# Kernel tuning notes

Hardware: AMD Instinct MI355X
Metric: run time of the kernel (lower is better)

## Reference

```python
import jax, jax.numpy as jnp
import numpy as np

COMMITMENT_COST = 0.25
EMBEDDING_DIM = 64
NUM_EMBEDDINGS = 512
BATCH, SEQ = 64, 4096


def setup_inputs() -> dict:
    key = jax.random.key(0)
    k1, k2, k3 = jax.random.split(key, 3)
    return {
        "inputs": jax.random.normal(k1, (BATCH, SEQ, EMBEDDING_DIM), dtype=jnp.float32),
        "embedding": jax.random.normal(k2, (NUM_EMBEDDINGS, EMBEDDING_DIM), dtype=jnp.float32),
        "ema_cluster_size": jax.random.uniform(k3, (NUM_EMBEDDINGS,), dtype=jnp.float32),
    }


def reference(inputs, embedding, ema_cluster_size):
    # inputs: [B, T, D]; embedding: [K, D]; ema_cluster_size: [K]
    input_shape = inputs.shape
    flat = inputs.reshape(-1, EMBEDDING_DIM)  # [N, D]
    distances = (
        jnp.sum(flat * flat, axis=1, keepdims=True)
        + jnp.sum(embedding * embedding, axis=1)[None, :]
        - 2.0 * (flat @ embedding.T)
    )
    # cluster-size weighting (as in the source module)
    distances = distances * jnp.sqrt(ema_cluster_size)[None, :]
    encoding_indices = jnp.argmin(distances, axis=1)  # [N]
    # one-hot @ codebook == gather
    quantized = embedding[encoding_indices].reshape(input_shape)
    e_latent_loss = jnp.mean((jax.lax.stop_gradient(quantized) - inputs) ** 2)
    loss = COMMITMENT_COST * e_latent_loss
    # straight-through estimator
    quantized_st = inputs + jax.lax.stop_gradient(quantized - inputs)
    return quantized_st, loss, encoding_indices[:, None]
```

## Files before the change

kernel.cpp:

```cpp
#include <hip/hip_runtime.h>
#include <math.h>

#define D 64
#define K 512

typedef __attribute__((ext_vector_type(8))) short short8;
typedef __attribute__((ext_vector_type(4))) float f32x4;

#define WS_E2    256
#define WS_SQ    2304
#define WS_ETS   4352
#define WS_BP    8448
#define WS_WL    139520
#define WS_PART  1188096
#define WS_PART2 1204480

#define KEYMASK 0xFFFFFE00u
#define DIST_BIAS 0.0625f

__device__ __forceinline__ unsigned short f32_to_bf16_rne(float f)
{
    unsigned int u = __float_as_uint(f);
    unsigned int r = (u + 0x7FFFu + ((u >> 16) & 1u)) >> 16;
    return (unsigned short)r;
}
__device__ __forceinline__ float bf16_to_f32(unsigned short h)
{
    return __uint_as_float(((unsigned int)h) << 16);
}

__device__ __forceinline__ float np_sumsq64(const float* v)
{
#pragma clang fp contract(off)
    float p[64];
#pragma unroll
    for (int i = 0; i < 64; ++i) p[i] = v[i] * v[i];
    float r[8];
#pragma unroll
    for (int j = 0; j < 8; ++j) r[j] = p[j];
#pragma unroll
    for (int b = 8; b < 64; b += 8) {
#pragma unroll
        for (int j = 0; j < 8; ++j) r[j] += p[b + j];
    }
    return ((r[0] + r[1]) + (r[2] + r[3])) + ((r[4] + r[5]) + (r[6] + r[7]));
}

__global__ __launch_bounds__(256) void vq_pack_prep(
    const float* __restrict__ emb,
    const float* __restrict__ cs,
    unsigned short* __restrict__ Bp,
    float* __restrict__ e2,
    float* __restrict__ sq,
    float2* __restrict__ ets,
    int* __restrict__ cnt)
{
    int i = blockIdx.x * blockDim.x + threadIdx.x;
    if (i < 65536) {
        int j    = i & 7;
        int lane = (i >> 3) & 63;
        int frag = (i >> 9) & 3;
        int t    = (i >> 11) & 31;
        int kc   = frag & 1;
        int sB   = frag >> 1;
        int code = t * 16 + (lane & 15);
        int d    = kc * 32 + (lane >> 4) * 8 + j;
        float v = emb[code * 64 + d];
        unsigned short b0 = f32_to_bf16_rne(v);
        Bp[i] = (sB == 0) ? b0 : f32_to_bf16_rne(v - bf16_to_f32(b0));
    } else if (i < 66048) {
        int k = i - 65536;
        float er[64];
        const float* ek = emb + (size_t)k * D;
#pragma unroll
        for (int d = 0; d < 64; ++d) er[d] = ek[d];
        float e2v = np_sumsq64(er);
        float sqv = (float)sqrt((double)cs[k]);
        e2[k] = e2v;
        sq[k] = sqv;
        ets[k] = make_float2(e2v * sqv + DIST_BIAS, 2.0f * sqv);
    } else if (i == 66048) {
        *cnt = 0;
    }
}

__global__ __launch_bounds__(256) void vq_screen(
    const float* __restrict__ x,
    const float* __restrict__ emb,
    const float2* __restrict__ ets,
    const unsigned short* __restrict__ Bp,
    float* __restrict__ out_q,
    float* __restrict__ out_idx,
    int* __restrict__ wl,
    int* __restrict__ cnt,
    double* __restrict__ partial)
{
    __shared__ double ls[4];

    const int wave = threadIdx.x >> 6;
    const int lane = threadIdx.x & 63;
    const int quad = lane >> 4;
    const int n16  = lane & 15;
    const int n0   = blockIdx.x * 128 + wave * 32;

    short8 A0[2][2], A1[2][2];
    float x2h[2][4];
#pragma unroll
    for (int rt = 0; rt < 2; ++rt) {
        float s = 0.0f;
#pragma unroll
        for (int kc = 0; kc < 2; ++kc) {
            const float* src = x + (size_t)(n0 + rt * 16 + n16) * 64
                               + kc * 32 + quad * 8;
            float4 v0 = *(const float4*)(src);
            float4 v1 = *(const float4*)(src + 4);
            float xv[8] = {v0.x, v0.y, v0.z, v0.w, v1.x, v1.y, v1.z, v1.w};
#pragma unroll
            for (int j = 0; j < 8; ++j) {
                float v = xv[j];
                unsigned short b0 = f32_to_bf16_rne(v);
                unsigned short b1 = f32_to_bf16_rne(v - bf16_to_f32(b0));
                A0[rt][kc][j] = (short)b0;
                A1[rt][kc][j] = (short)b1;
                s = fmaf(v, v, s);
            }
        }
        s += __shfl_xor(s, 16, 64);
        s += __shfl_xor(s, 32, 64);
#pragma unroll
        for (int r = 0; r < 4; ++r)
            x2h[rt][r] = 0.5f * __shfl(s, quad * 4 + r, 64);
    }

    unsigned k1[2][4], k2[2][4];
#pragma unroll
    for (int rt = 0; rt < 2; ++rt)
#pragma unroll
        for (int r = 0; r < 4; ++r) { k1[rt][r] = 0xFFFFFFFFu; k2[rt][r] = 0xFFFFFFFFu; }

#pragma unroll 2
    for (int t = 0; t < 32; ++t) {
        const unsigned short* bp = Bp + t * 2048 + lane * 8;
        const short8 B00 = *(const short8*)(bp);
        const short8 B01 = *(const short8*)(bp + 512);
        const short8 B10 = *(const short8*)(bp + 1024);
        const short8 B11 = *(const short8*)(bp + 1536);
        float2 et = ets[t * 16 + n16];
        unsigned cbits = (unsigned)(t * 16 + n16);

#pragma unroll
        for (int rt = 0; rt < 2; ++rt) {
            f32x4 acc = {0.0f, 0.0f, 0.0f, 0.0f};
            acc = __builtin_amdgcn_mfma_f32_16x16x32_bf16(A0[rt][0], B00, acc, 0, 0, 0);
            acc = __builtin_amdgcn_mfma_f32_16x16x32_bf16(A0[rt][1], B01, acc, 0, 0, 0);
            acc = __builtin_amdgcn_mfma_f32_16x16x32_bf16(A0[rt][0], B10, acc, 0, 0, 0);
            acc = __builtin_amdgcn_mfma_f32_16x16x32_bf16(A0[rt][1], B11, acc, 0, 0, 0);
            acc = __builtin_amdgcn_mfma_f32_16x16x32_bf16(A1[rt][0], B00, acc, 0, 0, 0);
            acc = __builtin_amdgcn_mfma_f32_16x16x32_bf16(A1[rt][1], B01, acc, 0, 0, 0);

#pragma unroll
            for (int r = 0; r < 4; ++r) {
                float dist = fmaf(x2h[rt][r], et.y, et.x);
                dist = fmaf(-et.y, acc[r], dist);
                unsigned key = (__float_as_uint(dist) & KEYMASK) | cbits;
                unsigned a1 = k1[rt][r];
                unsigned mx = a1 > key ? a1 : key;
                k1[rt][r] = a1 < key ? a1 : key;
                k2[rt][r] = k2[rt][r] < mx ? k2[rt][r] : mx;
            }
        }
    }

#pragma unroll
    for (int rt = 0; rt < 2; ++rt)
#pragma unroll
        for (int r = 0; r < 4; ++r) {
            unsigned a1 = k1[rt][r], a2 = k2[rt][r];
#pragma unroll
            for (int w = 1; w < 16; w <<= 1) {
                unsigned o1 = (unsigned)__shfl_xor((int)a1, w, 64);
                unsigned o2 = (unsigned)__shfl_xor((int)a2, w, 64);
                unsigned mx  = a1 > o1 ? a1 : o1;
                a1 = a1 < o1 ? a1 : o1;
                unsigned mn2 = a2 < o2 ? a2 : o2;
                a2 = mn2 < mx ? mn2 : mx;
            }
            k1[rt][r] = a1; k2[rt][r] = a2;
        }

    unsigned pk[2][4];
#pragma unroll
    for (int rt = 0; rt < 2; ++rt)
#pragma unroll
        for (int r = 0; r < 4; ++r) {
            float d1f = __uint_as_float(k1[rt][r] & KEYMASK);
            float d2f = __uint_as_float(k2[rt][r] & KEYMASK);
            int   i1  = (int)(k1[rt][r] & 0x1FFu);
            int   flg = (d2f - d1f) <= (0.01f + 2.0e-4f * d2f);
            pk[rt][r] = (unsigned)i1 | (flg ? 0x8000u : 0u);
            if (n16 == 0) {
                int p = n0 + rt * 16 + quad * 4 + r;
                out_idx[p] = (float)i1;
                if (flg) { int slot = atomicAdd(cnt, 1); wl[slot] = p; }
            }
        }

    int src = (n16 >> 2) * 16 + n16;
    double s = 0.0;
#pragma unroll
    for (int rt = 0; rt < 2; ++rt) {
        unsigned p0 = (unsigned)__shfl((int)pk[rt][0], src, 64);
        unsigned p1 = (unsigned)__shfl((int)pk[rt][1], src, 64);
        unsigned p2 = (unsigned)__shfl((int)pk[rt][2], src, 64);
        unsigned p3 = (unsigned)__shfl((int)pk[rt][3], src, 64);
        int rr = n16 & 3;
        unsigned pm = (rr == 0) ? p0 : (rr == 1) ? p1 : (rr == 2) ? p2 : p3;
        int bim = (int)(pm & 0x1FFu);
        int flg = (int)((pm >> 15) & 1u);
        if (!flg) {
            int prow = n0 + rt * 16 + n16;
#pragma unroll
            for (int kc = 0; kc < 2; ++kc) {
                const float* xs = x   + (size_t)prow * 64 + kc * 32 + quad * 8;
                const float* es = emb + (size_t)bim  * 64 + kc * 32 + quad * 8;
                float4 xv0 = *(const float4*)(xs);
                float4 xv1 = *(const float4*)(xs + 4);
                float4 ev0 = *(const float4*)(es);
                float4 ev1 = *(const float4*)(es + 4);
                float4 o0, o1;
                float t0, t1, t2, t3, t4, t5, t6, t7;
                {
#pragma clang fp contract(off)
                    t0 = ev0.x - xv0.x; o0.x = xv0.x + t0;
                    t1 = ev0.y - xv0.y; o0.y = xv0.y + t1;
                    t2 = ev0.z - xv0.z; o0.z = xv0.z + t2;
                    t3 = ev0.w - xv0.w; o0.w = xv0.w + t3;
                    t4 = ev1.x - xv1.x; o1.x = xv1.x + t4;
                    t5 = ev1.y - xv1.y; o1.y = xv1.y + t5;
                    t6 = ev1.z - xv1.z; o1.z = xv1.z + t6;
                    t7 = ev1.w - xv1.w; o1.w = xv1.w + t7;
                }
                float* od = out_q + (size_t)prow * 64 + kc * 32 + quad * 8;
                *(float4*)(od)     = o0;
                *(float4*)(od + 4) = o1;
                s += (double)t0 * t0 + (double)t1 * t1
                   + (double)t2 * t2 + (double)t3 * t3
                   + (double)t4 * t4 + (double)t5 * t5
                   + (double)t6 * t6 + (double)t7 * t7;
            }
        }
    }

#pragma unroll
    for (int off = 32; off > 0; off >>= 1)
        s += __shfl_down(s, off, 64);
    if (lane == 0) ls[wave] = s;
    __syncthreads();
    if (threadIdx.x == 0)
        partial[blockIdx.x] = ls[0] + ls[1] + ls[2] + ls[3];
}

__global__ __launch_bounds__(256) void vq_exact(
    const float* __restrict__ x,
    const float* __restrict__ emb,
    const float* __restrict__ e2,
    const float* __restrict__ sq,
    const int* __restrict__ wl,
    const int* __restrict__ cnt,
    float* __restrict__ out_idx,
    float* __restrict__ out_q,
    double* __restrict__ partial2)
{
    const int lane = threadIdx.x & 63;
    const int gw   = blockIdx.x * 4 + (threadIdx.x >> 6);
    const int nw   = gridDim.x * 4;
    const int cv   = *cnt;

    for (int w = gw; w < cv; w += nw) {
        int p = wl[w];
        const float* xrow = x + (size_t)p * 64;
        float row[64];
#pragma unroll
        for (int i = 0; i < 16; ++i) {
            float4 v = ((const float4*)xrow)[i];
            row[4 * i + 0] = v.x; row[4 * i + 1] = v.y;
            row[4 * i + 2] = v.z; row[4 * i + 3] = v.w;
        }
        float x2 = np_sumsq64(row);

        float bd = INFINITY;
        int   bc = 0;
        for (int t = 0; t < 8; ++t) {
            int c = t * 64 + lane;
            const float* er = emb + (size_t)c * 64;
            float acc = 0.0f;
#pragma unroll
            for (int d = 0; d < 64; ++d)
                acc = fmaf(row[d], er[d], acc);
            float dist;
            {
#pragma clang fp contract(off)
                dist = ((x2 + e2[c]) - 2.0f * acc) * sq[c];
            }
            if (dist < bd) { bd = dist; bc = c; }
        }
#pragma unroll
        for (int wd = 1; wd < 64; wd <<= 1) {
            float od = __shfl_xor(bd, wd, 64);
            int   oc = __shfl_xor(bc, wd, 64);
            if (od < bd || (od == bd && oc < bc)) { bd = od; bc = oc; }
        }
        if (lane == 0) out_idx[p] = (float)bc;

        float xv = x[(size_t)p * 64 + lane];
        float qv = emb[(size_t)bc * 64 + lane];
        float t, o;
        {
#pragma clang fp contract(off)
            t = qv - xv;
            o = xv + t;
        }
        out_q[(size_t)p * 64 + lane] = o;
        double dd = (double)t * (double)t;
#pragma unroll
        for (int off = 32; off > 0; off >>= 1)
            dd += __shfl_down(dd, off, 64);
        if (lane == 0) partial2[w] = dd;
    }
}

__global__ __launch_bounds__(256) void vq_finalize(
    const double* __restrict__ partial,
    const double* __restrict__ partial2,
    const int* __restrict__ cnt,
    float* __restrict__ loss_out,
    int nblk, double inv_count)
{
    double s = 0.0;
    for (int i = threadIdx.x; i < nblk; i += 256) s += partial[i];
    int cv = *cnt;
    for (int w = threadIdx.x; w < cv; w += 256) s += partial2[w];
#pragma unroll
    for (int off = 32; off > 0; off >>= 1)
        s += __shfl_down(s, off, 64);
    __shared__ double ls[4];
    if ((threadIdx.x & 63) == 0) ls[threadIdx.x >> 6] = s;
    __syncthreads();
    if (threadIdx.x == 0) {
        double total = ls[0] + ls[1] + ls[2] + ls[3];
        loss_out[0] = (float)(0.25 * total * inv_count);
    }
}

extern "C" void kernel_launch(void* const* d_in, const int* in_sizes, int n_in,
                              void* d_out, int out_size, void* d_ws, size_t ws_size,
                              hipStream_t stream)
{
    const float* x   = (const float*)d_in[0];
    const float* emb = (const float*)d_in[1];
    const float* cs  = (const float*)d_in[2];

    const int N = in_sizes[0] / D;

    float* out      = (float*)d_out;
    float* out_q    = out;
    float* out_loss = out + (size_t)N * D;
    float* out_idx  = out_loss + 1;

    char* ws = (char*)d_ws;
    int*            cnt      = (int*)ws;
    float*          e2       = (float*)(ws + WS_E2);
    float*          sq       = (float*)(ws + WS_SQ);
    float2*         ets      = (float2*)(ws + WS_ETS);
    unsigned short* Bp       = (unsigned short*)(ws + WS_BP);
    int*            wl       = (int*)(ws + WS_WL);
    double*         partial  = (double*)(ws + WS_PART);
    double*         partial2 = (double*)(ws + WS_PART2);

    const int nblk_screen = N / 128;

    vq_pack_prep<<<259, 256, 0, stream>>>(emb, cs, Bp, e2, sq, ets, cnt);
    vq_screen<<<nblk_screen, 256, 0, stream>>>(x, emb, ets, Bp,
                                               out_q, out_idx, wl, cnt, partial);
    vq_exact<<<512, 256, 0, stream>>>(x, emb, e2, sq, wl, cnt,
                                      out_idx, out_q, partial2);
    vq_finalize<<<1, 256, 0, stream>>>(partial, partial2, cnt, out_loss,
                                       nblk_screen, 1.0 / ((double)N * (double)D));
}
```

Baseline: 214.6 us.

## Stage packed codebook in LDS and process more rows per larger block

The screening kernel now copies the whole packed bf16 codebook (128 KB) into shared memory once per block and reads the MFMA B operands from LDS instead of global or L2. Blocks grow to 512 threads, each covering 512 rows in two passes, so the staging cost is amortised. It also seeds the accumulator with -x²/2 to drop one FMA and uses v_med3_u32 for the second-smallest key update. The 128 KB of LDS per block limits occupancy to one block per CU, and the staging copy plus barrier adds latency at the start of each block.

```diff
diff --git a/kernel.cpp b/kernel.cpp
--- a/kernel.cpp
+++ b/kernel.cpp
@@ -84,7 +84,7 @@
     }
 }
 
-__global__ __launch_bounds__(256) void vq_screen(
+__global__ __launch_bounds__(512) void vq_screen(
     const float* __restrict__ x,
     const float* __restrict__ emb,
     const float2* __restrict__ ets,
@@ -95,158 +95,173 @@
     int* __restrict__ cnt,
     double* __restrict__ partial)
 {
-    __shared__ double ls[4];
+    __shared__ unsigned short BpS[65536];
+    __shared__ double ls[8];
 
     const int wave = threadIdx.x >> 6;
     const int lane = threadIdx.x & 63;
     const int quad = lane >> 4;
     const int n16  = lane & 15;
-    const int n0   = blockIdx.x * 128 + wave * 32;
-
-    short8 A0[2][2], A1[2][2];
-    float x2h[2][4];
-#pragma unroll
-    for (int rt = 0; rt < 2; ++rt) {
-        float s = 0.0f;
-#pragma unroll
-        for (int kc = 0; kc < 2; ++kc) {
-            const float* src = x + (size_t)(n0 + rt * 16 + n16) * 64
-                               + kc * 32 + quad * 8;
-            float4 v0 = *(const float4*)(src);
-            float4 v1 = *(const float4*)(src + 4);
-            float xv[8] = {v0.x, v0.y, v0.z, v0.w, v1.x, v1.y, v1.z, v1.w};
-#pragma unroll
-            for (int j = 0; j < 8; ++j) {
-                float v = xv[j];
-                unsigned short b0 = f32_to_bf16_rne(v);
-                unsigned short b1 = f32_to_bf16_rne(v - bf16_to_f32(b0));
-                A0[rt][kc][j] = (short)b0;
-                A1[rt][kc][j] = (short)b1;
-                s = fmaf(v, v, s);
-            }
-        }
-        s += __shfl_xor(s, 16, 64);
-        s += __shfl_xor(s, 32, 64);
-#pragma unroll
-        for (int r = 0; r < 4; ++r)
-            x2h[rt][r] = 0.5f * __shfl(s, quad * 4 + r, 64);
-    }
-
-    unsigned k1[2][4], k2[2][4];
-#pragma unroll
-    for (int rt = 0; rt < 2; ++rt)
-#pragma unroll
-        for (int r = 0; r < 4; ++r) { k1[rt][r] = 0xFFFFFFFFu; k2[rt][r] = 0xFFFFFFFFu; }
+
+    {
+        const float4* src = (const float4*)Bp;
+        float4* dst = (float4*)BpS;
+#pragma unroll
+        for (int it = 0; it < 16; ++it)
+            dst[threadIdx.x + it * 512] = src[threadIdx.x + it * 512];
+    }
+    __syncthreads();
+
+    double s = 0.0;
+
+    for (int pass = 0; pass < 2; ++pass) {
+        const int n0 = blockIdx.x * 512 + pass * 256 + wave * 32;
+
+        short8 A0[2][2], A1[2][2];
+        f32x4 negx2h[2];
+#pragma unroll
+        for (int rt = 0; rt < 2; ++rt) {
+            float sx = 0.0f;
+#pragma unroll
+            for (int kc = 0; kc < 2; ++kc) {
+                const float* src = x + (size_t)(n0 + rt * 16 + n16) * 64
+                                   + kc * 32 + quad * 8;
+                float4 v0 = *(const float4*)(src);
+                float4 v1 = *(const float4*)(src + 4);
+                float xv[8] = {v0.x, v0.y, v0.z, v0.w, v1.x, v1.y, v1.z, v1.w};
+#pragma unroll
+                for (int j = 0; j < 8; ++j) {
+                    float v = xv[j];
+                    unsigned short b0 = f32_to_bf16_rne(v);
+                    unsigned short b1 = f32_to_bf16_rne(v - bf16_to_f32(b0));
+                    A0[rt][kc][j] = (short)b0;
+                    A1[rt][kc][j] = (short)b1;
+                    sx = fmaf(v, v, sx);
+                }
+            }
+            sx += __shfl_xor(sx, 16, 64);
+            sx += __shfl_xor(sx, 32, 64);
+#pragma unroll
+            for (int r = 0; r < 4; ++r)
+                negx2h[rt][r] = -0.5f * __shfl(sx, quad * 4 + r, 64);
+        }
+
+        unsigned k1[2][4], k2[2][4];
+#pragma unroll
+        for (int rt = 0; rt < 2; ++rt)
+#pragma unroll
+            for (int r = 0; r < 4; ++r) { k1[rt][r] = 0xFFFFFFFFu; k2[rt][r] = 0xFFFFFFFFu; }
 
 #pragma unroll 2
-    for (int t = 0; t < 32; ++t) {
-        const unsigned short* bp = Bp + t * 2048 + lane * 8;
-        const short8 B00 = *(const short8*)(bp);
-        const short8 B01 = *(const short8*)(bp + 512);
-        const short8 B10 = *(const short8*)(bp + 1024);
-        const short8 B11 = *(const short8*)(bp + 1536);
-        float2 et = ets[t * 16 + n16];
-        unsigned cbits = (unsigned)(t * 16 + n16);
-
+        for (int t = 0; t < 32; ++t) {
+            const unsigned short* bp = BpS + t * 2048 + lane * 8;
+            const short8 B00 = *(const short8*)(bp);
+            const short8 B01 = *(const short8*)(bp + 512);
+            const short8 B10 = *(const short8*)(bp + 1024);
+            const short8 B11 = *(const short8*)(bp + 1536);
+            float2 et = ets[t * 16 + n16];
+            unsigned cbits = (unsigned)(t * 16 + n16);
+
+#pragma unroll
+            for (int rt = 0; rt < 2; ++rt) {
+                f32x4 acc = negx2h[rt];
+                acc = __builtin_amdgcn_mfma_f32_16x16x32_bf16(A0[rt][0], B00, acc, 0, 0, 0);
+                acc = __builtin_amdgcn_mfma_f32_16x16x32_bf16(A0[rt][1], B01, acc, 0, 0, 0);
+                acc = __builtin_amdgcn_mfma_f32_16x16x32_bf16(A0[rt][0], B10, acc, 0, 0, 0);
+                acc = __builtin_amdgcn_mfma_f32_16x16x32_bf16(A0[rt][1], B11, acc, 0, 0, 0);
+                acc = __builtin_amdgcn_mfma_f32_16x16x32_bf16(A1[rt][0], B00, acc, 0, 0, 0);
+                acc = __builtin_amdgcn_mfma_f32_16x16x32_bf16(A1[rt][1], B01, acc, 0, 0, 0);
+
+#pragma unroll
+                for (int r = 0; r < 4; ++r) {
+                    float dist = fmaf(-et.y, acc[r], et.x);
+                    unsigned key = (__float_as_uint(dist) & KEYMASK) | cbits;
+                    unsigned a1 = k1[rt][r];
+                    unsigned a2;
+                    asm("v_med3_u32 %0, %1, %2, %3"
+                        : "=v"(a2) : "v"(a1), "v"(k2[rt][r]), "v"(key));
+                    k2[rt][r] = a2;
+                    k1[rt][r] = a1 < key ? a1 : key;
+                }
+            }
+        }
+
+#pragma unroll
+        for (int rt = 0; rt < 2; ++rt)
+#pragma unroll
+            for (int r = 0; r < 4; ++r) {
+                unsigned a1 = k1[rt][r], a2 = k2[rt][r];
+#pragma unroll
+                for (int w = 1; w < 16; w <<= 1) {
+                    unsigned o1 = (unsigned)__shfl_xor((int)a1, w, 64);
+                    unsigned o2 = (unsigned)__shfl_xor((int)a2, w, 64);
+                    unsigned mx  = a1 > o1 ? a1 : o1;
+                    a1 = a1 < o1 ? a1 : o1;
+                    unsigned mn2 = a2 < o2 ? a2 : o2;
+                    a2 = mn2 < mx ? mn2 : mx;
+                }
+                k1[rt][r] = a1; k2[rt][r] = a2;
+            }
+
+        unsigned pk[2][4];
+#pragma unroll
+        for (int rt = 0; rt < 2; ++rt)
+#pragma unroll
+            for (int r = 0; r < 4; ++r) {
+                float d1f = __uint_as_float(k1[rt][r] & KEYMASK);
+                float d2f = __uint_as_float(k2[rt][r] & KEYMASK);
+                int   i1  = (int)(k1[rt][r] & 0x1FFu);
+                int   flg = (d2f - d1f) <= (0.01f + 2.0e-4f * d2f);
+                pk[rt][r] = (unsigned)i1 | (flg ? 0x8000u : 0u);
+                if (n16 == 0) {
+                    int p = n0 + rt * 16 + quad * 4 + r;
+                    out_idx[p] = (float)i1;
+                    if (flg) { int slot = atomicAdd(cnt, 1); wl[slot] = p; }
+                }
+            }
+
+        int src = (n16 >> 2) * 16 + n16;
 #pragma unroll
         for (int rt = 0; rt < 2; ++rt) {
-            f32x4 acc = {0.0f, 0.0f, 0.0f, 0.0f};
-            acc = __builtin_amdgcn_mfma_f32_16x16x32_bf16(A0[rt][0], B00, acc, 0, 0, 0);
-            acc = __builtin_amdgcn_mfma_f32_16x16x32_bf16(A0[rt][1], B01, acc, 0, 0, 0);
-            acc = __builtin_amdgcn_mfma_f32_16x16x32_bf16(A0[rt][0], B10, acc, 0, 0, 0);
-            acc = __builtin_amdgcn_mfma_f32_16x16x32_bf16(A0[rt][1], B11, acc, 0, 0, 0);
-            acc = __builtin_amdgcn_mfma_f32_16x16x32_bf16(A1[rt][0], B00, acc, 0, 0, 0);
-            acc = __builtin_amdgcn_mfma_f32_16x16x32_bf16(A1[rt][1], B01, acc, 0, 0, 0);
-
-#pragma unroll
-            for (int r = 0; r < 4; ++r) {
-                float dist = fmaf(x2h[rt][r], et.y, et.x);
-                dist = fmaf(-et.y, acc[r], dist);
-                unsigned key = (__float_as_uint(dist) & KEYMASK) | cbits;
-                unsigned a1 = k1[rt][r];
-                unsigned mx = a1 > key ? a1 : key;
-                k1[rt][r] = a1 < key ? a1 : key;
-                k2[rt][r] = k2[rt][r] < mx ? k2[rt][r] : mx;
-            }
-        }
-    }
-
-#pragma unroll
-    for (int rt = 0; rt < 2; ++rt)
-#pragma unroll
-        for (int r = 0; r < 4; ++r) {
-            unsigned a1 = k1[rt][r], a2 = k2[rt][r];
-#pragma unroll
-            for (int w = 1; w < 16; w <<= 1) {
-                unsigned o1 = (unsigned)__shfl_xor((int)a1, w, 64);
-                unsigned o2 = (unsigned)__shfl_xor((int)a2, w, 64);
-                unsigned mx  = a1 > o1 ? a1 : o1;
-                a1 = a1 < o1 ? a1 : o1;
-                unsigned mn2 = a2 < o2 ? a2 : o2;
-                a2 = mn2 < mx ? mn2 : mx;
-            }
-            k1[rt][r] = a1; k2[rt][r] = a2;
-        }
-
-    unsigned pk[2][4];
-#pragma unroll
-    for (int rt = 0; rt < 2; ++rt)
-#pragma unroll
-        for (int r = 0; r < 4; ++r) {
-            float d1f = __uint_as_float(k1[rt][r] & KEYMASK);
-            float d2f = __uint_as_float(k2[rt][r] & KEYMASK);
-            int   i1  = (int)(k1[rt][r] & 0x1FFu);
-            int   flg = (d2f - d1f) <= (0.01f + 2.0e-4f * d2f);
-            pk[rt][r] = (unsigned)i1 | (flg ? 0x8000u : 0u);
-            if (n16 == 0) {
-                int p = n0 + rt * 16 + quad * 4 + r;
-                out_idx[p] = (float)i1;
-                if (flg) { int slot = atomicAdd(cnt, 1); wl[slot] = p; }
-            }
-        }
-
-    int src = (n16 >> 2) * 16 + n16;
-    double s = 0.0;
-#pragma unroll
-    for (int rt = 0; rt < 2; ++rt) {
-        unsigned p0 = (unsigned)__shfl((int)pk[rt][0], src, 64);
-        unsigned p1 = (unsigned)__shfl((int)pk[rt][1], src, 64);
-        unsigned p2 = (unsigned)__shfl((int)pk[rt][2], src, 64);
-        unsigned p3 = (unsigned)__shfl((int)pk[rt][3], src, 64);
-        int rr = n16 & 3;
-        unsigned pm = (rr == 0) ? p0 : (rr == 1) ? p1 : (rr == 2) ? p2 : p3;
-        int bim = (int)(pm & 0x1FFu);
-        int flg = (int)((pm >> 15) & 1u);
-        if (!flg) {
-            int prow = n0 + rt * 16 + n16;
-#pragma unroll
-            for (int kc = 0; kc < 2; ++kc) {
-                const float* xs = x   + (size_t)prow * 64 + kc * 32 + quad * 8;
-                const float* es = emb + (size_t)bim  * 64 + kc * 32 + quad * 8;
-                float4 xv0 = *(const float4*)(xs);
-                float4 xv1 = *(const float4*)(xs + 4);
-                float4 ev0 = *(const float4*)(es);
-                float4 ev1 = *(const float4*)(es + 4);
-                float4 o0, o1;
-                float t0, t1, t2, t3, t4, t5, t6, t7;
-                {
+            unsigned p0 = (unsigned)__shfl((int)pk[rt][0], src, 64);
+            unsigned p1 = (unsigned)__shfl((int)pk[rt][1], src, 64);
+            unsigned p2 = (unsigned)__shfl((int)pk[rt][2], src, 64);
+            unsigned p3 = (unsigned)__shfl((int)pk[rt][3], src, 64);
+            int rr = n16 & 3;
+            unsigned pm = (rr == 0) ? p0 : (rr == 1) ? p1 : (rr == 2) ? p2 : p3;
+            int bim = (int)(pm & 0x1FFu);
+            int flg = (int)((pm >> 15) & 1u);
+            if (!flg) {
+                int prow = n0 + rt * 16 + n16;
+#pragma unroll
+                for (int kc = 0; kc < 2; ++kc) {
+                    const float* xs = x   + (size_t)prow * 64 + kc * 32 + quad * 8;
+                    const float* es = emb + (size_t)bim  * 64 + kc * 32 + quad * 8;
+                    float4 xv0 = *(const float4*)(xs);
+                    float4 xv1 = *(const float4*)(xs + 4);
+                    float4 ev0 = *(const float4*)(es);
+                    float4 ev1 = *(const float4*)(es + 4);
+                    float4 o0, o1;
+                    float t0, t1, t2, t3, t4, t5, t6, t7;
+                    {
 #pragma clang fp contract(off)
-                    t0 = ev0.x - xv0.x; o0.x = xv0.x + t0;
-                    t1 = ev0.y - xv0.y; o0.y = xv0.y + t1;
-                    t2 = ev0.z - xv0.z; o0.z = xv0.z + t2;
-                    t3 = ev0.w - xv0.w; o0.w = xv0.w + t3;
-                    t4 = ev1.x - xv1.x; o1.x = xv1.x + t4;
-                    t5 = ev1.y - xv1.y; o1.y = xv1.y + t5;
-                    t6 = ev1.z - xv1.z; o1.z = xv1.z + t6;
-                    t7 = ev1.w - xv1.w; o1.w = xv1.w + t7;
+                        t0 = ev0.x - xv0.x; o0.x = xv0.x + t0;
+                        t1 = ev0.y - xv0.y; o0.y = xv0.y + t1;
+                        t2 = ev0.z - xv0.z; o0.z = xv0.z + t2;
+                        t3 = ev0.w - xv0.w; o0.w = xv0.w + t3;
+                        t4 = ev1.x - xv1.x; o1.x = xv1.x + t4;
+                        t5 = ev1.y - xv1.y; o1.y = xv1.y + t5;
+                        t6 = ev1.z - xv1.z; o1.z = xv1.z + t6;
+                        t7 = ev1.w - xv1.w; o1.w = xv1.w + t7;
+                    }
+                    float* od = out_q + (size_t)prow * 64 + kc * 32 + quad * 8;
+                    *(float4*)(od)     = o0;
+                    *(float4*)(od + 4) = o1;
+                    s += (double)t0 * t0 + (double)t1 * t1
+                       + (double)t2 * t2 + (double)t3 * t3
+                       + (double)t4 * t4 + (double)t5 * t5
+                       + (double)t6 * t6 + (double)t7 * t7;
                 }
-                float* od = out_q + (size_t)prow * 64 + kc * 32 + quad * 8;
-                *(float4*)(od)     = o0;
-                *(float4*)(od + 4) = o1;
-                s += (double)t0 * t0 + (double)t1 * t1
-                   + (double)t2 * t2 + (double)t3 * t3
-                   + (double)t4 * t4 + (double)t5 * t5
-                   + (double)t6 * t6 + (double)t7 * t7;
             }
         }
     }
@@ -257,7 +272,8 @@
     if (lane == 0) ls[wave] = s;
     __syncthreads();
     if (threadIdx.x == 0)
-        partial[blockIdx.x] = ls[0] + ls[1] + ls[2] + ls[3];
+        partial[blockIdx.x] = ls[0] + ls[1] + ls[2] + ls[3]
+                            + ls[4] + ls[5] + ls[6] + ls[7];
 }
 
 __global__ __launch_bounds__(256) void vq_exact(
@@ -377,10 +393,10 @@
     double*         partial  = (double*)(ws + WS_PART);
     double*         partial2 = (double*)(ws + WS_PART2);
 
-    const int nblk_screen = N / 128;
+    const int nblk_screen = N / 512;
 
     vq_pack_prep<<<259, 256, 0, stream>>>(emb, cs, Bp, e2, sq, ets, cnt);
-    vq_screen<<<nblk_screen, 256, 0, stream>>>(x, emb, ets, Bp,
+    vq_screen<<<nblk_screen, 512, 0, stream>>>(x, emb, ets, Bp,
                                                out_q, out_idx, wl, cnt, partial);
     vq_exact<<<512, 256, 0, stream>>>(x, emb, e2, sq, wl, cnt,
                                       out_idx, out_q, partial2);
```

Result: faster. 210.0 us (-2.1%).
